# Optimization experiments

Measured on AMD Instinct MI355X. Metric: run time of the kernel, lower is better.

## Reference

```python
import jax, jax.numpy as jnp
import numpy as np


def _h(s):
    # Step function: 0 where s > 0, else 1 (zero gradient everywhere).
    return jnp.where(s > 0, 0.0, 1.0).astype(s.dtype)


def setup_inputs() -> dict:
    key = jax.random.key(0)
    k1, k2, k3 = jax.random.split(key, 3)
    B, T = 4096, 2048
    x = jax.random.normal(k1, (B, T, 1), dtype=jnp.float32)
    out_prev = jax.random.normal(k2, (B, 1, 1), dtype=jnp.float32)
    lstm_outs = jax.random.normal(k3, (B, T, 4), dtype=jnp.float32)
    return {"x": x, "out_prev": out_prev, "lstm_outs": lstm_outs}


def reference(x, out_prev, lstm_outs):
    # x: [B, T, 1], out_prev: [B, 1, 1] (only first step used), lstm_outs: [B, T, 4]
    xT = jnp.swapaxes(x, 0, 1)          # [T, B, 1]
    wT = jnp.swapaxes(lstm_outs, 0, 1)  # [T, B, 4]

    def step(prev, inputs):
        # prev: [B, 1]
        xt, wt = inputs                  # [B, 1], [B, 4]
        m_lo = wt[:, 0:1]
        m_up = wt[:, 1:2]
        c_lo = wt[:, 2:3]
        c_up = wt[:, 3:4]
        # h() arguments use detached weights in the original (grad is zero through
        # the step function anyway); stop_gradient kept for faithfulness.
        m_lo_d = jax.lax.stop_gradient(m_lo)
        m_up_d = jax.lax.stop_gradient(m_up)
        c_lo_d = jax.lax.stop_gradient(c_lo)
        c_up_d = jax.lax.stop_gradient(c_up)
        f1 = _h((m_lo_d * xt + m_lo_d * c_lo_d - prev) / m_lo_d)
        f2 = _h((prev - m_up_d * xt - m_up_d * c_up_d) / m_up_d)
        out = (m_lo * xt * f1 + m_lo * c_lo * f1
               + m_up * xt * f2 + m_up * c_up * f2
               + prev * (1.0 - f1) * (1.0 - f2))
        return out, out

    init = out_prev[:, 0, :]             # [B, 1]
    _, outs = jax.lax.scan(step, init, (xT, wT))  # outs: [T, B, 1]
    custom_output = jnp.swapaxes(outs, 0, 1)      # [B, T, 1]
    # Original also returns (lstm_outs, 0, 0, 0) passthrough; main output is below.
    return custom_output
```

## Files before the change

### kernel.cpp

```cpp
#include <hip/hip_runtime.h>


#define C 64
#define NCH 32
#define NTB 3
#define NOB 4
#define TS 65
#define XS 68

#define CFENCE() asm volatile("" ::: "memory")

__global__ __launch_bounds__(192) void pc_scan(
    const float* __restrict__ x, const float* __restrict__ p0,
    const float4* __restrict__ lstm4, float* __restrict__ out,
    int B, int T) {
#pragma clang fp contract(off)
  __shared__ float4 tileA[NTB][16 * TS];
  __shared__ float4 tileB[NTB][16 * TS];
  __shared__ float xt[16 * XS];
  __shared__ float ostg[NOB][16 * XS];
  __shared__ int stagedw[2][NCH];
  __shared__ int scanned;

  const int tid = threadIdx.x;
  const int b0 = blockIdx.x * 16;
  const float4* x4 = reinterpret_cast<const float4*>(x);
  float4* out4 = reinterpret_cast<float4*>(out);

  for (int i = tid; i < 2 * NCH; i += 192) ((int*)stagedw)[i] = 0;
  if (tid == 0) scanned = 0;
  __syncthreads();

  if (tid >= 64) {
    const int q = tid - 64;
    const int pj = (q >> 3) & 15;
    const int pk = q & 7;
    const int w = (tid >> 6) - 1;
    const bool lead = (q & 63) == 0;

    float4 L00, L01, L02, L03, L04, L05, L06, L07;
    float4 L10, L11, L12, L13, L14, L15, L16, L17;
    float4 X00, X01, X10, X11;

#define ISSUE(S, CH)                                                    \
  {                                                                     \
    size_t rb = (size_t)(b0 + pj) * T + (size_t)(CH) * C;               \
    const float4* lp = lstm4 + rb + pk;                                 \
    L##S##0 = lp[0];  L##S##1 = lp[8];  L##S##2 = lp[16];               \
    L##S##3 = lp[24]; L##S##4 = lp[32]; L##S##5 = lp[40];               \
    L##S##6 = lp[48]; L##S##7 = lp[56];                                 \
    X##S##0 = x4[(rb >> 2) + 2 * pk];                                   \
    X##S##1 = x4[(rb >> 2) + 2 * pk + 1];                               \
  }

#define STAGE_ELT(LV, SS, BUF)                                          \
  {                                                                     \
    float4 wv = LV;                       \
    float xv = xt[pj * XS + (SS)];                                      \
    float a1 = wv.x * xv, a2 = wv.x * wv.z;                             \
    float L1v = a1 + a2;                                                \
    unsigned s1m = __float_as_uint(wv.x) & 0x80000000u;                 \
    float L1f = __uint_as_float(__float_as_uint(L1v) ^ s1m);            \
    float a3 = wv.y * xv, a4 = wv.y * wv.w;                             \
    unsigned f2m = (__float_as_uint(wv.y) & 0x80000000u) ^ 0x80000000u; \
    float a3f = __uint_as_float(__float_as_uint(a3) ^ f2m);             \
    float a4f = __uint_as_float(__float_as_uint(a4) ^ f2m);             \
    float V01 = a3 + a4;                                                \
    float V11 = (L1v + a3) + a4;                                        \
    tileA[BUF][pj * TS + (SS)] =                                        \
        make_float4(__uint_as_float(s1m), L1f, __uint_as_float(f2m), a3f); \
    tileB[BUF][pj * TS + (SS)] = make_float4(a4f, V11, V01, L1v);       \
  }

#define STAGE(S, BUF)                                                   \
  {                                                                     \
    *(float4*)&xt[pj * XS + 8 * pk] = X##S##0;                          \
    *(float4*)&xt[pj * XS + 8 * pk + 4] = X##S##1;                      \
    STAGE_ELT(L##S##0, pk,      BUF)                                    \
    STAGE_ELT(L##S##1, pk + 8,  BUF)                                    \
    STAGE_ELT(L##S##2, pk + 16, BUF)                                    \
    STAGE_ELT(L##S##3, pk + 24, BUF)                                    \
    STAGE_ELT(L##S##4, pk + 32, BUF)                                    \
    STAGE_ELT(L##S##5, pk + 40, BUF)                                    \
    STAGE_ELT(L##S##6, pk + 48, BUF)                                    \
    STAGE_ELT(L##S##7, pk + 56, BUF)                                    \
  }

#define FLUSH(CP, OB)                                                   \
  {                                                                     \
    float4 v0 = *(const float4*)&ostg[OB][pj * XS + 8 * pk];            \
    float4 v1 = *(const float4*)&ostg[OB][pj * XS + 8 * pk + 4];        \
    size_t ob = ((size_t)(b0 + pj) * T + (size_t)(CP) * C) >> 2;        \
    out4[ob + 2 * pk] = v0;                                             \
    out4[ob + 2 * pk + 1] = v1;                                         \
  }

#define PWAIT(TGT)                                                      \
  while (*(volatile int*)&scanned < (TGT)) __builtin_amdgcn_s_sleep(1); \
  CFENCE();

    ISSUE(0, 0)
    ISSUE(1, 1)

    for (int k = 0; k < NCH; k += 2) {
      PWAIT(k - 2)
      STAGE(0, k % NTB)
      CFENCE();
      if (lead) *(volatile int*)&stagedw[w][k] = 1;
      if (k + 2 < NCH) ISSUE(0, k + 2)
      if (k >= 3) FLUSH(k - 3, (k - 3) % NOB)
      PWAIT(k - 1)
      STAGE(1, (k + 1) % NTB)
      CFENCE();
      if (lead) *(volatile int*)&stagedw[w][k + 1] = 1;
      if (k + 3 < NCH) ISSUE(1, k + 3)
      if (k >= 2) FLUSH(k - 2, (k - 2) % NOB)
    }
    for (int j = NCH - 3; j < NCH; ++j) {
      PWAIT(j + 1)
      FLUSH(j, j % NOB)
    }
  } else {
    float p = (tid < 16) ? p0[b0 + tid] : 0.0f;

#define RSTEP(I, OVC)                                                   \
  {                                                                     \
    float4 A = rA##I;                                                   \
    float4 Bv = rB##I;                                                  \
    if (g < 7) {                                                        \
      rA##I = ta[8 * g + 8 + I];                                        \
      rB##I = tb[8 * g + 8 + I];                                        \
    }                                                                   \
    unsigned pu = __float_as_uint(p);                                   \
    float pf = __uint_as_float(pu ^ __float_as_uint(A.x));              \
    bool c1 = pf >= A.y;                                                \
    float pp = __uint_as_float(pu ^ __float_as_uint(A.z));              \
    float qv = pp - A.w;                                                \
    bool c2 = qv >= Bv.x;                                               \
    float i1 = c1 ? Bv.y : Bv.z;                                        \
    float i2 = c1 ? Bv.w : p;                                           \
    p = c2 ? i1 : i2;                                                   \
    OVC = p;                                                            \
  }

    for (int c = 0; c < NCH; ++c) {
      for (;;) {
        int a = *(volatile int*)&stagedw[0][c];
        int b = *(volatile int*)&stagedw[1][c];
        if (a + b == 2) break;
        __builtin_amdgcn_s_sleep(1);
      }
      CFENCE();
      if (tid < 16) {
        const float4* ta = &tileA[c % NTB][tid * TS];
        const float4* tb = &tileB[c % NTB][tid * TS];
        float* orow = &ostg[c % NOB][tid * XS];
        float4 rA0 = ta[0], rA1 = ta[1], rA2 = ta[2], rA3 = ta[3];
        float4 rA4 = ta[4], rA5 = ta[5], rA6 = ta[6], rA7 = ta[7];
        float4 rB0 = tb[0], rB1 = tb[1], rB2 = tb[2], rB3 = tb[3];
        float4 rB4 = tb[4], rB5 = tb[5], rB6 = tb[6], rB7 = tb[7];
#pragma unroll
        for (int g = 0; g < 8; ++g) {
          float4 ov0, ov1;
          RSTEP(0, ov0.x) RSTEP(1, ov0.y) RSTEP(2, ov0.z) RSTEP(3, ov0.w)
          RSTEP(4, ov1.x) RSTEP(5, ov1.y) RSTEP(6, ov1.z) RSTEP(7, ov1.w)
          *(float4*)&orow[8 * g] = ov0;
          *(float4*)&orow[8 * g + 4] = ov1;
        }
      }
      CFENCE();
      if (tid == 0) *(volatile int*)&scanned = c + 1;
    }
  }
}

extern "C" void kernel_launch(void* const* d_in, const int* in_sizes, int n_in,
                              void* d_out, int out_size, void* d_ws, size_t ws_size,
                              hipStream_t stream) {
  const float* x = (const float*)d_in[0];
  const float* op = (const float*)d_in[1];
  const float4* lstm = (const float4*)d_in[2];
  int B = in_sizes[1];
  int T = in_sizes[0] / B;
  hipLaunchKernelGGL(pc_scan, dim3(B / 16), dim3(192), 0, stream,
                     x, op, lstm, (float*)d_out, B, T);
}
```

Measured before the change: 230.6 us.

## Scan 32 rows per block with 32-step chunks and counter-based handshakes

Result: slower. 264.4 us (+14.7%).

```diff
diff --git a/kernel.cpp b/kernel.cpp
--- a/kernel.cpp
+++ b/kernel.cpp
@@ -1,12 +1,13 @@
 #include <hip/hip_runtime.h>
 
 
-#define C 64
-#define NCH 32
+#define C 32
+#define NCH 64
 #define NTB 3
 #define NOB 4
-#define TS 65
-#define XS 68
+#define TSP 33
+#define OSP 33
+#define RPB 32
 
 #define CFENCE() asm volatile("" ::: "memory")
 
@@ -15,48 +16,56 @@
     const float4* __restrict__ lstm4, float* __restrict__ out,
     int B, int T) {
 #pragma clang fp contract(off)
-  __shared__ float4 tileA[NTB][16 * TS];
-  __shared__ float4 tileB[NTB][16 * TS];
-  __shared__ float xt[16 * XS];
-  __shared__ float ostg[NOB][16 * XS];
-  __shared__ int stagedw[2][NCH];
+  __shared__ float4 tileA[NTB][RPB * TSP];
+  __shared__ float4 tileB[NTB][RPB * TSP];
+  __shared__ float xt[RPB * OSP];
+  __shared__ float ostg[NOB][RPB * OSP];
+  __shared__ int staged[2];
   __shared__ int scanned;
 
   const int tid = threadIdx.x;
-  const int b0 = blockIdx.x * 16;
+  const int b0 = blockIdx.x * RPB;
   const float4* x4 = reinterpret_cast<const float4*>(x);
   float4* out4 = reinterpret_cast<float4*>(out);
 
-  for (int i = tid; i < 2 * NCH; i += 192) ((int*)stagedw)[i] = 0;
-  if (tid == 0) scanned = 0;
+  if (tid == 0) { staged[0] = 0; staged[1] = 0; scanned = 0; }
   __syncthreads();
 
   if (tid >= 64) {
-    const int q = tid - 64;
-    const int pj = (q >> 3) & 15;
-    const int pk = q & 7;
-    const int w = (tid >> 6) - 1;
-    const bool lead = (q & 63) == 0;
+    const int pw = (tid >> 6) - 1;
+    const int l = tid & 63;
+    const int sph = l & 7;
+    const int lr0 = 16 * pw + (l >> 3);
+    const int lr1 = lr0 + 8;
+    const size_t gr0 = (size_t)(b0 + lr0) * T;
+    const size_t gr1 = (size_t)(b0 + lr1) * T;
 
-    float4 L00, L01, L02, L03, L04, L05, L06, L07;
-    float4 L10, L11, L12, L13, L14, L15, L16, L17;
-    float4 X00, X01, X10, X11;
+    float4 La0, La1, La2, La3, La4, La5, La6, La7, Xa0, Xa1;
+    float4 Lb0, Lb1, Lb2, Lb3, Lb4, Lb5, Lb6, Lb7, Xb0, Xb1;
+    int scc = 0;
+
+#define PWAIT(TGT)                                                      \
+  if (scc < (TGT)) {                                                    \
+    while ((scc = *(volatile int*)&scanned) < (TGT))                    \
+      __builtin_amdgcn_s_sleep(1);                                      \
+  }                                                                     \
+  CFENCE();
 
 #define ISSUE(S, CH)                                                    \
   {                                                                     \
-    size_t rb = (size_t)(b0 + pj) * T + (size_t)(CH) * C;               \
-    const float4* lp = lstm4 + rb + pk;                                 \
-    L##S##0 = lp[0];  L##S##1 = lp[8];  L##S##2 = lp[16];               \
-    L##S##3 = lp[24]; L##S##4 = lp[32]; L##S##5 = lp[40];               \
-    L##S##6 = lp[48]; L##S##7 = lp[56];                                 \
-    X##S##0 = x4[(rb >> 2) + 2 * pk];                                   \
-    X##S##1 = x4[(rb >> 2) + 2 * pk + 1];                               \
+    size_t t0 = (size_t)(CH) * C;                                       \
+    const float4* q0 = lstm4 + gr0 + t0 + sph;                          \
+    const float4* q1 = lstm4 + gr1 + t0 + sph;                          \
+    L##S##0 = q0[0]; L##S##1 = q0[8]; L##S##2 = q0[16]; L##S##3 = q0[24];\
+    L##S##4 = q1[0]; L##S##5 = q1[8]; L##S##6 = q1[16]; L##S##7 = q1[24];\
+    X##S##0 = x4[((gr0 + t0) >> 2) + sph];                              \
+    X##S##1 = x4[((gr1 + t0) >> 2) + sph];                              \
   }
 
-#define STAGE_ELT(LV, SS, BUF)                                          \
+#define STAGE_ELT(LV, LR, SS, SLOT)                                     \
   {                                                                     \
     float4 wv = LV;                       \
-    float xv = xt[pj * XS + (SS)];                                      \
+    float xv = xt[(LR)*OSP + (SS)];                                     \
     float a1 = wv.x * xv, a2 = wv.x * wv.z;                             \
     float L1v = a1 + a2;                                                \
     unsigned s1m = __float_as_uint(wv.x) & 0x80000000u;                 \
@@ -67,67 +76,64 @@
     float a4f = __uint_as_float(__float_as_uint(a4) ^ f2m);             \
     float V01 = a3 + a4;                                                \
     float V11 = (L1v + a3) + a4;                                        \
-    tileA[BUF][pj * TS + (SS)] =                                        \
+    tileA[SLOT][(LR)*TSP + (SS)] =                                      \
         make_float4(__uint_as_float(s1m), L1f, __uint_as_float(f2m), a3f); \
-    tileB[BUF][pj * TS + (SS)] = make_float4(a4f, V11, V01, L1v);       \
+    tileB[SLOT][(LR)*TSP + (SS)] = make_float4(a4f, V11, V01, L1v);     \
   }
 
-#define STAGE(S, BUF)                                                   \
+#define STAGE(S, SLOT)                                                  \
   {                                                                     \
-    *(float4*)&xt[pj * XS + 8 * pk] = X##S##0;                          \
-    *(float4*)&xt[pj * XS + 8 * pk + 4] = X##S##1;                      \
-    STAGE_ELT(L##S##0, pk,      BUF)                                    \
-    STAGE_ELT(L##S##1, pk + 8,  BUF)                                    \
-    STAGE_ELT(L##S##2, pk + 16, BUF)                                    \
-    STAGE_ELT(L##S##3, pk + 24, BUF)                                    \
-    STAGE_ELT(L##S##4, pk + 32, BUF)                                    \
-    STAGE_ELT(L##S##5, pk + 40, BUF)                                    \
-    STAGE_ELT(L##S##6, pk + 48, BUF)                                    \
-    STAGE_ELT(L##S##7, pk + 56, BUF)                                    \
+    *(float4*)&xt[lr0 * OSP + 4 * sph] = X##S##0;                       \
+    *(float4*)&xt[lr1 * OSP + 4 * sph] = X##S##1;                       \
+    STAGE_ELT(L##S##0, lr0, sph + 0,  SLOT)                             \
+    STAGE_ELT(L##S##1, lr0, sph + 8,  SLOT)                             \
+    STAGE_ELT(L##S##2, lr0, sph + 16, SLOT)                             \
+    STAGE_ELT(L##S##3, lr0, sph + 24, SLOT)                             \
+    STAGE_ELT(L##S##4, lr1, sph + 0,  SLOT)                             \
+    STAGE_ELT(L##S##5, lr1, sph + 8,  SLOT)                             \
+    STAGE_ELT(L##S##6, lr1, sph + 16, SLOT)                             \
+    STAGE_ELT(L##S##7, lr1, sph + 24, SLOT)                             \
   }
 
 #define FLUSH(CP, OB)                                                   \
   {                                                                     \
-    float4 v0 = *(const float4*)&ostg[OB][pj * XS + 8 * pk];            \
-    float4 v1 = *(const float4*)&ostg[OB][pj * XS + 8 * pk + 4];        \
-    size_t ob = ((size_t)(b0 + pj) * T + (size_t)(CP) * C) >> 2;        \
-    out4[ob + 2 * pk] = v0;                                             \
-    out4[ob + 2 * pk + 1] = v1;                                         \
+    float4 v0 = *(const float4*)&ostg[OB][lr0 * OSP + 4 * sph];         \
+    float4 v1 = *(const float4*)&ostg[OB][lr1 * OSP + 4 * sph];         \
+    size_t t0 = (size_t)(CP) * C;                                       \
+    out4[((gr0 + t0) >> 2) + sph] = v0;                                 \
+    out4[((gr1 + t0) >> 2) + sph] = v1;                                 \
   }
 
-#define PWAIT(TGT)                                                      \
-  while (*(volatile int*)&scanned < (TGT)) __builtin_amdgcn_s_sleep(1); \
-  CFENCE();
-
-    ISSUE(0, 0)
-    ISSUE(1, 1)
+    ISSUE(a, 0)
+    ISSUE(b, 1)
 
     for (int k = 0; k < NCH; k += 2) {
       PWAIT(k - 2)
-      STAGE(0, k % NTB)
+      STAGE(a, k % NTB)
       CFENCE();
-      if (lead) *(volatile int*)&stagedw[w][k] = 1;
-      if (k + 2 < NCH) ISSUE(0, k + 2)
-      if (k >= 3) FLUSH(k - 3, (k - 3) % NOB)
+      if (l == 0) *(volatile int*)&staged[pw] = k + 1;
+      if (k + 2 < NCH) ISSUE(a, k + 2)
+      if (k >= 3) FLUSH(k - 3, (k - 3) & (NOB - 1))
+
       PWAIT(k - 1)
-      STAGE(1, (k + 1) % NTB)
+      STAGE(b, (k + 1) % NTB)
       CFENCE();
-      if (lead) *(volatile int*)&stagedw[w][k + 1] = 1;
-      if (k + 3 < NCH) ISSUE(1, k + 3)
-      if (k >= 2) FLUSH(k - 2, (k - 2) % NOB)
+      if (l == 0) *(volatile int*)&staged[pw] = k + 2;
+      if (k + 3 < NCH) ISSUE(b, k + 3)
+      if (k >= 2) FLUSH(k - 2, (k - 2) & (NOB - 1))
     }
-    for (int j = NCH - 3; j < NCH; ++j) {
-      PWAIT(j + 1)
-      FLUSH(j, j % NOB)
-    }
+    PWAIT(NCH - 2) FLUSH(NCH - 3, (NCH - 3) & (NOB - 1))
+    PWAIT(NCH - 1) FLUSH(NCH - 2, (NCH - 2) & (NOB - 1))
+    PWAIT(NCH)     FLUSH(NCH - 1, (NCH - 1) & (NOB - 1))
   } else {
-    float p = (tid < 16) ? p0[b0 + tid] : 0.0f;
+    float p = (tid < RPB) ? p0[b0 + tid] : 0.0f;
+    int st0 = 0, st1 = 0;
 
 #define RSTEP(I, OVC)                                                   \
   {                                                                     \
     float4 A = rA##I;                                                   \
     float4 Bv = rB##I;                                                  \
-    if (g < 7) {                                                        \
+    if (g < 3) {                                                        \
       rA##I = ta[8 * g + 8 + I];                                        \
       rB##I = tb[8 * g + 8 + I];                                        \
     }                                                                   \
@@ -144,28 +150,32 @@
   }
 
     for (int c = 0; c < NCH; ++c) {
-      for (;;) {
-        int a = *(volatile int*)&stagedw[0][c];
-        int b = *(volatile int*)&stagedw[1][c];
-        if (a + b == 2) break;
-        __builtin_amdgcn_s_sleep(1);
+      if (st0 < c + 1 || st1 < c + 1) {
+        do {
+          st0 = *(volatile int*)&staged[0];
+          st1 = *(volatile int*)&staged[1];
+        } while (st0 < c + 1 || st1 < c + 1);
       }
       CFENCE();
-      if (tid < 16) {
-        const float4* ta = &tileA[c % NTB][tid * TS];
-        const float4* tb = &tileB[c % NTB][tid * TS];
-        float* orow = &ostg[c % NOB][tid * XS];
-        float4 rA0 = ta[0], rA1 = ta[1], rA2 = ta[2], rA3 = ta[3];
-        float4 rA4 = ta[4], rA5 = ta[5], rA6 = ta[6], rA7 = ta[7];
-        float4 rB0 = tb[0], rB1 = tb[1], rB2 = tb[2], rB3 = tb[3];
-        float4 rB4 = tb[4], rB5 = tb[5], rB6 = tb[6], rB7 = tb[7];
+      {
+        const int slot = c % NTB;
+        const int ob = c & (NOB - 1);
+        if (tid < RPB) {
+          const float4* ta = &tileA[slot][tid * TSP];
+          const float4* tb = &tileB[slot][tid * TSP];
+          float* orow = &ostg[ob][tid * OSP];
+          float4 rA0 = ta[0], rA1 = ta[1], rA2 = ta[2], rA3 = ta[3];
+          float4 rA4 = ta[4], rA5 = ta[5], rA6 = ta[6], rA7 = ta[7];
+          float4 rB0 = tb[0], rB1 = tb[1], rB2 = tb[2], rB3 = tb[3];
+          float4 rB4 = tb[4], rB5 = tb[5], rB6 = tb[6], rB7 = tb[7];
 #pragma unroll
-        for (int g = 0; g < 8; ++g) {
-          float4 ov0, ov1;
-          RSTEP(0, ov0.x) RSTEP(1, ov0.y) RSTEP(2, ov0.z) RSTEP(3, ov0.w)
-          RSTEP(4, ov1.x) RSTEP(5, ov1.y) RSTEP(6, ov1.z) RSTEP(7, ov1.w)
-          *(float4*)&orow[8 * g] = ov0;
-          *(float4*)&orow[8 * g + 4] = ov1;
+          for (int g = 0; g < 4; ++g) {
+            float4 ov0, ov1;
+            RSTEP(0, ov0.x) RSTEP(1, ov0.y) RSTEP(2, ov0.z) RSTEP(3, ov0.w)
+            RSTEP(4, ov1.x) RSTEP(5, ov1.y) RSTEP(6, ov1.z) RSTEP(7, ov1.w)
+            *(float4*)&orow[8 * g] = ov0;
+            *(float4*)&orow[8 * g + 4] = ov1;
+          }
         }
       }
       CFENCE();
@@ -182,6 +192,6 @@
   const float4* lstm = (const float4*)d_in[2];
   int B = in_sizes[1];
   int T = in_sizes[0] / B;
-  hipLaunchKernelGGL(pc_scan, dim3(B / 16), dim3(192), 0, stream,
+  hipLaunchKernelGGL(pc_scan, dim3(B / RPB), dim3(192), 0, stream,
                      x, op, lstm, (float*)d_out, B, T);
 }
```
